# Kernel optimization log

Measured on AMD Instinct MI355X. Metric: run time of the kernel, lower is better.

Reference implementation:

```python
import jax, jax.numpy as jnp
import numpy as np
import math

L, B, T, S, D, H = 6, 4, 1024, 1024, 1024, 16
HD = D // H
SCALE = 1.0 / math.sqrt(HD)
EPS = 1e-5


def _ln(x, w, b):
    m = x.mean(-1, keepdims=True)
    v = ((x - m) ** 2).mean(-1, keepdims=True)
    return (x - m) * jax.lax.rsqrt(v + EPS) * w + b


def _mha(xq, xkv, qw, qb, kw, kb, vw, vb, ow, ob, mask):
    b, t, _ = xq.shape
    s = xkv.shape[1]
    q = (xq @ qw.T + qb).reshape(b, t, H, HD).transpose(0, 2, 1, 3)
    k = (xkv @ kw.T + kb).reshape(b, s, H, HD).transpose(0, 2, 1, 3)
    v = (xkv @ vw.T + vb).reshape(b, s, H, HD).transpose(0, 2, 1, 3)
    scores = jnp.einsum('bhqd,bhkd->bhqk', q, k) * SCALE
    scores = jnp.where(mask == 0, -jnp.inf, scores)
    attn = jax.nn.softmax(scores, axis=-1)  # dropout is identity (eval)
    o = jnp.einsum('bhqk,bhkd->bhqd', attn, v).transpose(0, 2, 1, 3).reshape(b, t, D)
    return o @ ow.T + ob


def _ffn(x, f1w, f1b, f2w, f2b, fnw, fnb):
    h = jax.nn.gelu(x @ f1w.T + f1b, approximate=False)
    y = h @ f2w.T + f2b
    return x + _ln(y, fnw, fnb)


def setup_inputs() -> dict:
    key = jax.random.key(0)
    ks = jax.random.split(key, 16)
    wf = lambda k: jax.random.normal(k, (L, D, D), jnp.float32) * 0.02
    zb = jnp.zeros((L, D), jnp.float32)
    ones = jnp.ones((L, D), jnp.float32)
    inp = {
        'x': jax.random.normal(ks[0], (B, T, D), jnp.float32),
        'enc_outputs': jax.random.normal(ks[1], (B, S, D), jnp.float32),
        'sqw': wf(ks[2]), 'sqb': zb, 'skw': wf(ks[3]), 'skb': zb,
        'svw': wf(ks[4]), 'svb': zb, 'sow': wf(ks[5]), 'sob': zb,
        'cqw': wf(ks[6]), 'cqb': zb, 'ckw': wf(ks[7]), 'ckb': zb,
        'cvw': wf(ks[8]), 'cvb': zb, 'cow': wf(ks[9]), 'cob': zb,
        'f1w': wf(ks[10]), 'f1b': zb, 'f2w': wf(ks[11]), 'f2b': zb,
        'fnw': ones, 'fnb': zb,
        'l1w': ones, 'l1b': zb, 'l2w': ones, 'l2b': zb, 'l3w': ones, 'l3b': zb,
        'src_mask': jnp.ones((1, 1, T, S), jnp.int32),
        'tgt_mask': jnp.tril(jnp.ones((T, T), jnp.int32))[None, None],
    }
    return inp


def reference(x, enc_outputs, sqw, sqb, skw, skb, svw, svb, sow, sob,
              cqw, cqb, ckw, ckb, cvw, cvb, cow, cob,
              f1w, f1b, f2w, f2b, fnw, fnb,
              l1w, l1b, l2w, l2b, l3w, l3b, src_mask, tgt_mask):
    for l in range(L):
        sa = _mha(x, x, sqw[l], sqb[l], skw[l], skb[l], svw[l], svb[l], sow[l], sob[l], tgt_mask)
        x = _ln(x + sa, l1w[l], l1b[l])
        ca = _mha(x, enc_outputs, cqw[l], cqb[l], ckw[l], ckb[l], cvw[l], cvb[l], cow[l], cob[l], src_mask)
        x = _ln(x + ca, l2w[l], l2b[l])
        ff = _ffn(x, f1w[l], f1b[l], f2w[l], f2b[l], fnw[l], fnb[l])
        x = _ln(x + ff, l3w[l], l3b[l])
    return x
```

## Files before the change

kernel.cpp:

```cpp
#include <hip/hip_runtime.h>
#include <stdint.h>

typedef unsigned short u16;
typedef unsigned int u32;
typedef __bf16 bf16x8 __attribute__((ext_vector_type(8)));
typedef float f32x4 __attribute__((ext_vector_type(4)));
typedef u16 u16x8 __attribute__((ext_vector_type(8)));
typedef u16 u16x4 __attribute__((ext_vector_type(4)));
typedef u32 u32x2 __attribute__((ext_vector_type(2)));

#define MFMA16(A, B, C) __builtin_amdgcn_mfma_f32_16x16x32_bf16((A), (B), (C), 0, 0, 0)

#define GLOAD_LDS16(GP, LP)                                                    \
  __builtin_amdgcn_global_load_lds(                                            \
      (__attribute__((address_space(1))) void*)(GP),                           \
      (__attribute__((address_space(3))) void*)(LP), 16, 0, 0)

__device__ __forceinline__ u16 f2bf(float f) {
  return __builtin_bit_cast(u16, (__bf16)f);
}

__device__ __forceinline__ float bf2f(u16 v) {
  return __builtin_bit_cast(float, ((u32)v) << 16);
}

__device__ __forceinline__ float exp2_raw(float x) {
  float r;
  asm("v_exp_f32 %0, %1\n\ts_nop 0" : "=v"(r) : "v"(x));
  return r;
}

__device__ __forceinline__ float max3f(float a, float b, float c) {
  float d;
  asm("v_max3_f32 %0, %1, %2, %3" : "=v"(d) : "v"(a), "v"(b), "v"(c));
  return d;
}

__device__ __forceinline__ u32 cvt_pk_bf16(float lo, float hi) {
  u32 r;
  asm("v_cvt_pk_bf16_f32 %0, %1, %2" : "=v"(r) : "v"(lo), "v"(hi));
  return r;
}

#define SC2 0.1803368801111204f
#define DEFER_THR 11.541560327f

struct WPtrs {
  const float* p[10];
};

__global__ __launch_bounds__(256) void wcvt_kernel(WPtrs w, u16* __restrict__ dst, int loff) {
  const int mat = blockIdx.y;
  const int i = blockIdx.x * 256 + threadIdx.x;
  float4 v = ((const float4*)(w.p[mat] + loff))[i];
  u16x4 o = {f2bf(v.x), f2bf(v.y), f2bf(v.z), f2bf(v.w)};
  ((u16x4*)dst)[(size_t)mat * gridDim.x * 256 + i] = o;
}

struct GemmArgs {
  const u16* A[3];
  const u16* W[3];
  const float* bias[3];
  u16* C[3];
  float scale[3];
};

__global__ __launch_bounds__(256, 4) void gemm_bt(GemmArgs g) {
  const int mat = blockIdx.y >> 3;
  const int n0 = (blockIdx.y & 7) * 128;
  const int m0 = blockIdx.x * 128;
  const int kz = blockIdx.z;
  const int kn = 16 / gridDim.z;
  const u16* __restrict__ A = g.A[mat];
  const u16* __restrict__ W = g.W[mat];

  __shared__ u16 As[128][64];
  __shared__ u16 Bs[128][64];

  const int tid = threadIdx.x;
  const int lane = tid & 63;
  const int wv = tid >> 6;
  const int wm = (wv >> 1) * 64;
  const int wn = (wv & 1) * 64;
  const int fr = lane & 15;
  const int fg = lane >> 4;

  f32x4 acc[4][4];
#pragma unroll
  for (int i = 0; i < 4; ++i)
#pragma unroll
    for (int j = 0; j < 4; ++j)
#pragma unroll
      for (int r = 0; r < 4; ++r) acc[i][j][r] = 0.f;

  const int row8 = lane >> 3;
  const int csw = ((lane & 7) ^ row8) * 8;
  const u16* ga = A + (size_t)(m0 + wv * 32 + row8) * 1024 + csw + kz * kn * 64;
  const u16* gb = W + (size_t)(n0 + wv * 32 + row8) * 1024 + csw + kz * kn * 64;

  for (int kt = 0; kt < kn; ++kt) {
    __syncthreads();
#pragma unroll
    for (int i = 0; i < 4; ++i) {
      GLOAD_LDS16(ga + (size_t)i * 8 * 1024, &As[wv * 32 + i * 8][0]);
      GLOAD_LDS16(gb + (size_t)i * 8 * 1024, &Bs[wv * 32 + i * 8][0]);
    }
    ga += 64;
    gb += 64;
    __syncthreads();
#pragma unroll
    for (int ks = 0; ks < 2; ++ks) {
      bf16x8 af[4], bfr[4];
#pragma unroll
      for (int i = 0; i < 4; ++i) {
        af[i] = *(const bf16x8*)&As[wm + i * 16 + fr][((ks * 4 + fg) ^ (fr & 7)) * 8];
        bfr[i] = *(const bf16x8*)&Bs[wn + i * 16 + fr][((ks * 4 + fg) ^ (fr & 7)) * 8];
      }
#pragma unroll
      for (int mi = 0; mi < 4; ++mi)
#pragma unroll
        for (int ni = 0; ni < 4; ++ni) acc[mi][ni] = MFMA16(af[mi], bfr[ni], acc[mi][ni]);
    }
  }

  const float* __restrict__ bias = g.bias[mat];
  const float scl = g.scale[mat];
  float bv[4];
#pragma unroll
  for (int ni = 0; ni < 4; ++ni) bv[ni] = (kz == 0) ? bias[n0 + wn + ni * 16 + fr] : 0.f;

  u16* __restrict__ C = g.C[mat] + (size_t)kz * (4096 * 1024);
#pragma unroll
  for (int mi = 0; mi < 4; ++mi) {
#pragma unroll
    for (int ni = 0; ni < 4; ++ni) {
      const int col = n0 + wn + ni * 16 + fr;
#pragma unroll
      for (int r = 0; r < 4; ++r) {
        const int row = m0 + wm + mi * 16 + fg * 4 + r;
        C[(size_t)row * 1024 + col] = f2bf((acc[mi][ni][r] + bv[ni]) * scl);
      }
    }
  }
}

__global__ __launch_bounds__(512, 4) void attn_fwd(const u16* __restrict__ Q,
                                                   const u16* __restrict__ K,
                                                   const u16* __restrict__ V,
                                                   u16* __restrict__ O, int causal) {
  const int b = blockIdx.x >> 4;
  const int h = blockIdx.x & 15;
  const int qb = causal ? (7 - blockIdx.y) : blockIdx.y;
  const int tid = threadIdx.x;
  const int lane = tid & 63;
  const int wv = tid >> 6;
  const int fr = lane & 15;
  const int fg = lane >> 4;

  __shared__ u16 Ks[2][64][64];
  __shared__ u16 Vt[2][64][64];
  __shared__ u16 Plds[8][16][64];

  const int qrow0 = b * 1024 + qb * 128 + wv * 16;
  const int col0 = h * 64;

  const u16* qp = Q + (size_t)(qrow0 + fr) * 1024 + col0 + fg * 8;
  bf16x8 aQ0 = *(const bf16x8*)qp;
  bf16x8 aQ1 = *(const bf16x8*)(qp + 32);

  f32x4 ov[4];
#pragma unroll
  for (int i = 0; i < 4; ++i)
#pragma unroll
    for (int r = 0; r < 4; ++r) ov[i][r] = 0.f;
  float m_run = -1e30f, l_part = 0.f;

  const int kv_base = b * 1024;
  const int qg = qb * 128 + wv * 16 + fr;
  const int nt = causal ? (2 * qb + 2) : 16;

  const u16* gk0 = K + (size_t)(kv_base + wv * 16 + (lane >> 3)) * 1024 + col0 +
                   (((lane & 7) ^ (lane >> 3)) * 8);
  const int vt = tid - 256;
  const int kkp = vt & 31;
  const int d0 = (vt >> 5) * 8;
  const u16* gv0 = V + (size_t)(kv_base + 2 * kkp) * 1024 + col0 + d0;

#define STAGE_K(T, BUF)                                                        \
  if (wv < 4) {                                                                \
    const u16* gk = gk0 + (size_t)(T)*64 * 1024;                               \
    GLOAD_LDS16(gk, &Ks[BUF][wv * 16][0]);                                     \
    GLOAD_LDS16(gk + 8 * 1024, &Ks[BUF][wv * 16 + 8][0]);                      \
  }
#define LOAD_V(T)                                                              \
  if (tid >= 256) {                                                            \
    const u16* gvp = gv0 + (size_t)(T)*64 * 1024;                              \
    vr0 = *(const u16x8*)gvp;                                                  \
    vr1 = *(const u16x8*)(gvp + 1024);                                         \
  }
#define WRITE_V(BUF)                                                           \
  if (tid >= 256) {                                                            \
    _Pragma("unroll") for (int j = 0; j < 8; ++j) {                            \
      u32 pk = (u32)vr0[j] | ((u32)vr1[j] << 16);                              \
      *(u32*)&Vt[BUF][d0 + j][(((kkp >> 2) ^ j) * 8) + (kkp & 3) * 2] = pk;    \
    }                                                                          \
  }

  u16x8 vr0, vr1;
  STAGE_K(0, 0);
  LOAD_V(0);
  WRITE_V(0);

  for (int t = 0; t < nt; ++t) {
    const int cur = t & 1;
    __syncthreads();
    const bool pf = (t + 1 < nt);
    if (pf) {
      STAGE_K(t + 1, cur ^ 1);
      LOAD_V(t + 1);
    }

    f32x4 st[4];
    __builtin_amdgcn_s_setprio(1);
#pragma unroll
    for (int hh = 0; hh < 4; ++hh) {
#pragma unroll
      for (int r = 0; r < 4; ++r) st[hh][r] = 0.f;
      const u16* krow = &Ks[cur][hh * 16 + fr][0];
      bf16x8 k0 = *(const bf16x8*)(krow + ((fg ^ (fr & 7)) * 8));
      bf16x8 k1 = *(const bf16x8*)(krow + (((4 + fg) ^ (fr & 7)) * 8));
      st[hh] = MFMA16(k0, aQ0, st[hh]);
      st[hh] = MFMA16(k1, aQ1, st[hh]);
    }
    __builtin_amdgcn_s_setprio(0);

    if (causal && t >= 2 * qb) {
#pragma unroll
      for (int hh = 0; hh < 4; ++hh)
#pragma unroll
        for (int r = 0; r < 4; ++r) {
          const int kkg = t * 64 + hh * 16 + fg * 4 + r;
          if (kkg > qg) st[hh][r] = -1e30f;
        }
    }

    float a = max3f(st[0][0], st[0][1], st[0][2]);
    a = max3f(a, st[0][3], st[1][0]);
    a = max3f(a, st[1][1], st[1][2]);
    a = max3f(a, st[1][3], st[2][0]);
    float bb = max3f(st[2][1], st[2][2], st[2][3]);
    bb = max3f(bb, st[3][0], st[3][1]);
    bb = max3f(bb, st[3][2], st[3][3]);
    const float tmax = fmaxf(a, bb);

    if (!__all(tmax <= m_run + DEFER_THR)) {
      float cm = fmaxf(tmax, __shfl_xor(tmax, 16));
      cm = fmaxf(cm, __shfl_xor(cm, 32));
      const float mnew = fmaxf(m_run, cm);
      const float fsc = exp2_raw(m_run - mnew);
      l_part *= fsc;
      float frs[4];
#pragma unroll
      for (int r = 0; r < 4; ++r) frs[r] = __shfl(fsc, fg * 4 + r);
#pragma unroll
      for (int dt = 0; dt < 4; ++dt)
#pragma unroll
        for (int r = 0; r < 4; ++r) ov[dt][r] *= frs[r];
      m_run = mnew;
    }

    float p[16];
#pragma unroll
    for (int hh = 0; hh < 4; ++hh)
#pragma unroll
      for (int r = 0; r < 4; ++r) {
        const float e = exp2_raw(st[hh][r] - m_run);
        p[hh * 4 + r] = e;
        l_part += e;
      }

#pragma unroll
    for (int hh = 0; hh < 4; ++hh) {
      u32x2 wpair = {cvt_pk_bf16(p[hh * 4 + 0], p[hh * 4 + 1]),
                     cvt_pk_bf16(p[hh * 4 + 2], p[hh * 4 + 3])};
      const int c = hh * 2 + (fg >> 1);
      *(u32x2*)&Plds[wv][fr][((c ^ (fr & 7)) * 8) + (fg & 1) * 4] = wpair;
    }
    bf16x8 pa[2];
#pragma unroll
    for (int ks = 0; ks < 2; ++ks)
      pa[ks] = *(const bf16x8*)&Plds[wv][fr][(((ks * 4 + fg) ^ (fr & 7)) * 8)];
    __builtin_amdgcn_s_setprio(1);
#pragma unroll
    for (int dt = 0; dt < 4; ++dt) {
#pragma unroll
      for (int ks = 0; ks < 2; ++ks) {
        bf16x8 bvv = *(const bf16x8*)&Vt[cur][dt * 16 + fr][(((ks * 4 + fg) ^ (fr & 7)) * 8)];
        ov[dt] = MFMA16(pa[ks], bvv, ov[dt]);
      }
    }
    __builtin_amdgcn_s_setprio(0);

    if (pf) WRITE_V(cur ^ 1);
  }

  float ps = l_part;
  ps += __shfl_xor(ps, 16);
  ps += __shfl_xor(ps, 32);
  const float linv = 1.0f / ps;
  float fin[4];
#pragma unroll
  for (int r = 0; r < 4; ++r) fin[r] = __shfl(linv, fg * 4 + r);
#pragma unroll
  for (int dt = 0; dt < 4; ++dt)
#pragma unroll
    for (int r = 0; r < 4; ++r) {
      const int row = qrow0 + fg * 4 + r;
      const int col = col0 + dt * 16 + fr;
      O[(size_t)row * 1024 + col] = f2bf(ov[dt][r] * fin[r]);
    }
#undef STAGE_K
#undef LOAD_V
#undef WRITE_V
}

__device__ __forceinline__ float4 ld_bf4(const u16* p, size_t idx4) {
  u16x4 t = ((const u16x4*)p)[idx4];
  return make_float4(bf2f(t[0]), bf2f(t[1]), bf2f(t[2]), bf2f(t[3]));
}

__global__ __launch_bounds__(256) void ln_res_kernel(const u16* __restrict__ Xb_in,
                                                     const u16* __restrict__ T0,
                                                     const u16* __restrict__ T1, int nT,
                                                     const float* __restrict__ w,
                                                     const float* __restrict__ bia,
                                                     u16* __restrict__ Xb_out) {
  __shared__ float red[2][4];
  const int row = blockIdx.x;
  const int tid = threadIdx.x;
  const int lane = tid & 63, wv = tid >> 6;
  const size_t base4 = (size_t)row * 256;
  float4 xv = ld_bf4(Xb_in, base4 + tid);
  float4 tv = ld_bf4(T0, base4 + tid);
  float z0 = xv.x + tv.x, z1 = xv.y + tv.y, z2 = xv.z + tv.z, z3 = xv.w + tv.w;
  if (nT == 2) {
    float4 t1 = ld_bf4(T1, base4 + tid);
    z0 += t1.x; z1 += t1.y; z2 += t1.z; z3 += t1.w;
  }
  float s = z0 + z1 + z2 + z3;
  float ss = z0 * z0 + z1 * z1 + z2 * z2 + z3 * z3;
#pragma unroll
  for (int m = 1; m <= 32; m <<= 1) {
    s += __shfl_xor(s, m);
    ss += __shfl_xor(ss, m);
  }
  if (lane == 0) {
    red[0][wv] = s;
    red[1][wv] = ss;
  }
  __syncthreads();
  s = red[0][0] + red[0][1] + red[0][2] + red[0][3];
  ss = red[1][0] + red[1][1] + red[1][2] + red[1][3];
  const float mean = s * (1.f / 1024.f);
  const float var = ss * (1.f / 1024.f) - mean * mean;
  const float rs = rsqrtf(fmaxf(var, 0.f) + 1e-5f);
  float4 wv4 = ((const float4*)w)[tid];
  float4 bv4 = ((const float4*)bia)[tid];
  float o0 = (z0 - mean) * rs * wv4.x + bv4.x;
  float o1 = (z1 - mean) * rs * wv4.y + bv4.y;
  float o2 = (z2 - mean) * rs * wv4.z + bv4.z;
  float o3 = (z3 - mean) * rs * wv4.w + bv4.w;
  u16x4 ob = {f2bf(o0), f2bf(o1), f2bf(o2), f2bf(o3)};
  ((u16x4*)Xb_out)[base4 + tid] = ob;
}

__global__ __launch_bounds__(256) void ffn_ln_kernel(
    const u16* __restrict__ Xb, const u16* __restrict__ Y0, const u16* __restrict__ Y1,
    int nT, const float* __restrict__ fw_, const float* __restrict__ fb_,
    const float* __restrict__ w3, const float* __restrict__ b3, u16* __restrict__ Xb_out,
    float* __restrict__ Fout) {
  __shared__ float red[2][4];
  const int row = blockIdx.x;
  const int tid = threadIdx.x;
  const int lane = tid & 63, wv = tid >> 6;
  const size_t base4 = (size_t)row * 256;
  float4 yv = ld_bf4(Y0, base4 + tid);
  if (nT == 2) {
    float4 y1 = ld_bf4(Y1, base4 + tid);
    yv.x += y1.x; yv.y += y1.y; yv.z += y1.z; yv.w += y1.w;
  }
  float s = yv.x + yv.y + yv.z + yv.w;
  float ss = yv.x * yv.x + yv.y * yv.y + yv.z * yv.z + yv.w * yv.w;
#pragma unroll
  for (int m = 1; m <= 32; m <<= 1) {
    s += __shfl_xor(s, m);
    ss += __shfl_xor(ss, m);
  }
  if (lane == 0) {
    red[0][wv] = s;
    red[1][wv] = ss;
  }
  __syncthreads();
  s = red[0][0] + red[0][1] + red[0][2] + red[0][3];
  ss = red[1][0] + red[1][1] + red[1][2] + red[1][3];
  const float mean = s * (1.f / 1024.f);
  const float var = ss * (1.f / 1024.f) - mean * mean;
  const float rs = rsqrtf(fmaxf(var, 0.f) + 1e-5f);
  float4 xv = ld_bf4(Xb, base4 + tid);
  float4 fw4 = ((const float4*)fw_)[tid];
  float4 fb4 = ((const float4*)fb_)[tid];
  float z0 = 2.f * xv.x + (yv.x - mean) * rs * fw4.x + fb4.x;
  float z1 = 2.f * xv.y + (yv.y - mean) * rs * fw4.y + fb4.y;
  float z2 = 2.f * xv.z + (yv.z - mean) * rs * fw4.z + fb4.z;
  float z3 = 2.f * xv.w + (yv.w - mean) * rs * fw4.w + fb4.w;
  float s2 = z0 + z1 + z2 + z3;
  float ss2 = z0 * z0 + z1 * z1 + z2 * z2 + z3 * z3;
#pragma unroll
  for (int m = 1; m <= 32; m <<= 1) {
    s2 += __shfl_xor(s2, m);
    ss2 += __shfl_xor(ss2, m);
  }
  __syncthreads();
  if (lane == 0) {
    red[0][wv] = s2;
    red[1][wv] = ss2;
  }
  __syncthreads();
  s2 = red[0][0] + red[0][1] + red[0][2] + red[0][3];
  ss2 = red[1][0] + red[1][1] + red[1][2] + red[1][3];
  const float mean2 = s2 * (1.f / 1024.f);
  const float var2 = ss2 * (1.f / 1024.f) - mean2 * mean2;
  const float rs2 = rsqrtf(fmaxf(var2, 0.f) + 1e-5f);
  float4 w4 = ((const float4*)w3)[tid];
  float4 b4 = ((const float4*)b3)[tid];
  float o0 = (z0 - mean2) * rs2 * w4.x + b4.x;
  float o1 = (z1 - mean2) * rs2 * w4.y + b4.y;
  float o2 = (z2 - mean2) * rs2 * w4.z + b4.z;
  float o3 = (z3 - mean2) * rs2 * w4.w + b4.w;
  u16x4 ob = {f2bf(o0), f2bf(o1), f2bf(o2), f2bf(o3)};
  ((u16x4*)Xb_out)[base4 + tid] = ob;
  if (Fout) ((float4*)Fout)[base4 + tid] = make_float4(o0, o1, o2, o3);
}

__global__ __launch_bounds__(256) void gelu_combine(const u16* __restrict__ T0,
                                                    const u16* __restrict__ T1, int nT,
                                                    u16* __restrict__ dst) {
  const size_t i = (size_t)blockIdx.x * 256 + threadIdx.x;
  float4 v = ld_bf4(T0, i);
  if (nT == 2) {
    float4 u = ld_bf4(T1, i);
    v.x += u.x; v.y += u.y; v.z += u.z; v.w += u.w;
  }
  v.x = 0.5f * v.x * (1.0f + erff(v.x * 0.70710678118654752f));
  v.y = 0.5f * v.y * (1.0f + erff(v.y * 0.70710678118654752f));
  v.z = 0.5f * v.z * (1.0f + erff(v.z * 0.70710678118654752f));
  v.w = 0.5f * v.w * (1.0f + erff(v.w * 0.70710678118654752f));
  u16x4 o = {f2bf(v.x), f2bf(v.y), f2bf(v.z), f2bf(v.w)};
  ((u16x4*)dst)[i] = o;
}

__global__ __launch_bounds__(256) void cast_kernel(const float* __restrict__ in,
                                                   u16* __restrict__ outb) {
  const size_t i = (size_t)blockIdx.x * 256 + threadIdx.x;
  float4 v = ((const float4*)in)[i];
  u16x4 o = {f2bf(v.x), f2bf(v.y), f2bf(v.z), f2bf(v.w)};
  ((u16x4*)outb)[i] = o;
}

extern "C" void kernel_launch(void* const* d_in, const int* in_sizes, int n_in, void* d_out,
                              int out_size, void* d_ws, size_t ws_size, hipStream_t stream) {
  const float* x_in = (const float*)d_in[0];
  const float* enc = (const float*)d_in[1];
  const float* sqw = (const float*)d_in[2];
  const float* sqb = (const float*)d_in[3];
  const float* skw = (const float*)d_in[4];
  const float* skb = (const float*)d_in[5];
  const float* svw = (const float*)d_in[6];
  const float* svb = (const float*)d_in[7];
  const float* sow = (const float*)d_in[8];
  const float* sob = (const float*)d_in[9];
  const float* cqw = (const float*)d_in[10];
  const float* cqb = (const float*)d_in[11];
  const float* ckw = (const float*)d_in[12];
  const float* ckb = (const float*)d_in[13];
  const float* cvw = (const float*)d_in[14];
  const float* cvb = (const float*)d_in[15];
  const float* cow = (const float*)d_in[16];
  const float* cob = (const float*)d_in[17];
  const float* f1w = (const float*)d_in[18];
  const float* f1b = (const float*)d_in[19];
  const float* f2w = (const float*)d_in[20];
  const float* f2b = (const float*)d_in[21];
  const float* fnw = (const float*)d_in[22];
  const float* fnb = (const float*)d_in[23];
  const float* l1w = (const float*)d_in[24];
  const float* l1b = (const float*)d_in[25];
  const float* l2w = (const float*)d_in[26];
  const float* l2b = (const float*)d_in[27];
  const float* l3w = (const float*)d_in[28];
  const float* l3b = (const float*)d_in[29];

  const size_t MB = 1024 * 1024;
  const int ALLW = (ws_size >= 200 * MB) ? 1 : 0;
  const int NS = (ws_size >= 90 * MB) ? 2 : 1;
  char* ws = (char*)d_ws;
  u16* tmpb = (u16*)ws;
  char* p = ws + (size_t)NS * 8 * MB;
  u16* xb = (u16*)p;   p += 8 * MB;
  u16* encb = (u16*)p; p += 8 * MB;
  u16* qbuf = (u16*)p; p += 8 * MB;
  u16* kbuf = (u16*)p; p += 8 * MB;
  u16* vbuf = (u16*)p; p += 8 * MB;
  u16* wbf = (u16*)p;
  u16* tmpb1 = tmpb + (size_t)4 * 1024 * 1024;
  const size_t W1M = 1024 * 1024;

  cast_kernel<<<4096, 256, 0, stream>>>(x_in, xb);
  cast_kernel<<<4096, 256, 0, stream>>>(enc, encb);

  WPtrs wp;
  wp.p[0] = sqw; wp.p[1] = skw; wp.p[2] = svw; wp.p[3] = sow;
  wp.p[4] = cqw; wp.p[5] = ckw; wp.p[6] = cvw; wp.p[7] = cow;
  wp.p[8] = f1w; wp.p[9] = f2w;

  if (ALLW) wcvt_kernel<<<dim3(6144, 10), 256, 0, stream>>>(wp, wbf, 0);

  for (int l = 0; l < 6; ++l) {
    const size_t bo = (size_t)l * 1024;
    if (!ALLW) wcvt_kernel<<<dim3(1024, 10), 256, 0, stream>>>(wp, wbf, l * (int)W1M);
    #define WT(t) (ALLW ? (wbf + ((size_t)(t)*6 + l) * W1M) : (wbf + (size_t)(t)*W1M))

    GemmArgs g;
    g.scale[0] = SC2; g.scale[1] = 1.f; g.scale[2] = 1.f;
    g.A[0] = xb; g.A[1] = xb; g.A[2] = xb;
    g.W[0] = WT(0); g.W[1] = WT(1); g.W[2] = WT(2);
    g.bias[0] = sqb + bo; g.bias[1] = skb + bo; g.bias[2] = svb + bo;
    g.C[0] = qbuf; g.C[1] = kbuf; g.C[2] = vbuf;
    gemm_bt<<<dim3(32, 24, 1), 256, 0, stream>>>(g);
    attn_fwd<<<dim3(64, 8), 512, 0, stream>>>(qbuf, kbuf, vbuf, qbuf, 1);
    g.scale[0] = 1.f;
    g.A[0] = qbuf; g.W[0] = WT(3); g.bias[0] = sob + bo; g.C[0] = tmpb;
    gemm_bt<<<dim3(32, 8, NS), 256, 0, stream>>>(g);
    ln_res_kernel<<<4096, 256, 0, stream>>>(xb, tmpb, tmpb1, NS, l1w + bo, l1b + bo, xb);

    g.scale[0] = SC2;
    g.A[0] = xb; g.A[1] = encb; g.A[2] = encb;
    g.W[0] = WT(4); g.W[1] = WT(5); g.W[2] = WT(6);
    g.bias[0] = cqb + bo; g.bias[1] = ckb + bo; g.bias[2] = cvb + bo;
    g.C[0] = qbuf; g.C[1] = kbuf; g.C[2] = vbuf;
    gemm_bt<<<dim3(32, 24, 1), 256, 0, stream>>>(g);
    attn_fwd<<<dim3(64, 8), 512, 0, stream>>>(qbuf, kbuf, vbuf, qbuf, 0);
    g.scale[0] = 1.f;
    g.A[0] = qbuf; g.W[0] = WT(7); g.bias[0] = cob + bo; g.C[0] = tmpb;
    gemm_bt<<<dim3(32, 8, NS), 256, 0, stream>>>(g);
    ln_res_kernel<<<4096, 256, 0, stream>>>(xb, tmpb, tmpb1, NS, l2w + bo, l2b + bo, xb);

    g.A[0] = xb; g.W[0] = WT(8); g.bias[0] = f1b + bo; g.C[0] = tmpb;
    gemm_bt<<<dim3(32, 8, NS), 256, 0, stream>>>(g);
    gelu_combine<<<4096, 256, 0, stream>>>(tmpb, tmpb1, NS, kbuf);
    g.A[0] = kbuf; g.W[0] = WT(9); g.bias[0] = f2b + bo; g.C[0] = tmpb;
    gemm_bt<<<dim3(32, 8, NS), 256, 0, stream>>>(g);
    float* fo = (l == 5) ? (float*)d_out : nullptr;
    ffn_ln_kernel<<<4096, 256, 0, stream>>>(xb, tmpb, tmpb1, NS, fnw + bo, fnb + bo, l3w + bo,
                                            l3b + bo, xb, fo);
    #undef WT
  }
}
```

Before: 1.352 ms.

## Rework attention to 4 waves of 32 query rows using 32x32 MFMA for QK^T

The attention kernel now runs 256 threads (4 waves), each wave owning 32 query rows instead of 16. QK^T uses the 32x32x16 bf16 MFMA, and each V fragment read from LDS feeds two 16x16 MFMAs, which halves LDS traffic per FLOP and drops the shuffle-based row max across lane groups. All threads now share K and V staging, and launch bounds change to (256,3). The weight-cast kernel is also widened to convert 16 floats per thread with fewer blocks. The cost is higher register pressure per wave and fewer waves in flight to hide latency.

```diff
diff --git a/kernel.cpp b/kernel.cpp
--- a/kernel.cpp
+++ b/kernel.cpp
@@ -5,11 +5,13 @@
 typedef unsigned int u32;
 typedef __bf16 bf16x8 __attribute__((ext_vector_type(8)));
 typedef float f32x4 __attribute__((ext_vector_type(4)));
+typedef float f32x16 __attribute__((ext_vector_type(16)));
 typedef u16 u16x8 __attribute__((ext_vector_type(8)));
 typedef u16 u16x4 __attribute__((ext_vector_type(4)));
 typedef u32 u32x2 __attribute__((ext_vector_type(2)));
 
 #define MFMA16(A, B, C) __builtin_amdgcn_mfma_f32_16x16x32_bf16((A), (B), (C), 0, 0, 0)
+#define MFMA32(A, B, C) __builtin_amdgcn_mfma_f32_32x32x16_bf16((A), (B), (C), 0, 0, 0)
 
 #define GLOAD_LDS16(GP, LP)                                                    \
   __builtin_amdgcn_global_load_lds(                                            \
@@ -51,10 +53,16 @@
 
 __global__ __launch_bounds__(256) void wcvt_kernel(WPtrs w, u16* __restrict__ dst, int loff) {
   const int mat = blockIdx.y;
-  const int i = blockIdx.x * 256 + threadIdx.x;
-  float4 v = ((const float4*)(w.p[mat] + loff))[i];
-  u16x4 o = {f2bf(v.x), f2bf(v.y), f2bf(v.z), f2bf(v.w)};
-  ((u16x4*)dst)[(size_t)mat * gridDim.x * 256 + i] = o;
+  const size_t t = (size_t)blockIdx.x * 256 + threadIdx.x;
+  const float4* src = (const float4*)(w.p[mat] + loff) + t * 4;
+  float4 v0 = src[0], v1 = src[1], v2 = src[2], v3 = src[3];
+  u16x8 o0 = {f2bf(v0.x), f2bf(v0.y), f2bf(v0.z), f2bf(v0.w),
+              f2bf(v1.x), f2bf(v1.y), f2bf(v1.z), f2bf(v1.w)};
+  u16x8 o1 = {f2bf(v2.x), f2bf(v2.y), f2bf(v2.z), f2bf(v2.w),
+              f2bf(v3.x), f2bf(v3.y), f2bf(v3.z), f2bf(v3.w)};
+  u16x8* d = (u16x8*)dst + (size_t)mat * gridDim.x * 512 + t * 2;
+  d[0] = o0;
+  d[1] = o1;
 }
 
 struct GemmArgs {
@@ -144,7 +152,7 @@
   }
 }
 
-__global__ __launch_bounds__(512, 4) void attn_fwd(const u16* __restrict__ Q,
+__global__ __launch_bounds__(256, 3) void attn_fwd(const u16* __restrict__ Q,
                                                    const u16* __restrict__ K,
                                                    const u16* __restrict__ V,
                                                    u16* __restrict__ O, int causal) {
@@ -156,50 +164,54 @@
   const int wv = tid >> 6;
   const int fr = lane & 15;
   const int fg = lane >> 4;
+  const int lq = lane & 31;
+  const int hi = lane >> 5;
 
   __shared__ u16 Ks[2][64][64];
   __shared__ u16 Vt[2][64][64];
-  __shared__ u16 Plds[8][16][64];
-
-  const int qrow0 = b * 1024 + qb * 128 + wv * 16;
+  __shared__ u16 Plds[4][32][64];
+
+  const int qrow0 = b * 1024 + qb * 128 + wv * 32;
   const int col0 = h * 64;
 
-  const u16* qp = Q + (size_t)(qrow0 + fr) * 1024 + col0 + fg * 8;
-  bf16x8 aQ0 = *(const bf16x8*)qp;
-  bf16x8 aQ1 = *(const bf16x8*)(qp + 32);
-
-  f32x4 ov[4];
-#pragma unroll
-  for (int i = 0; i < 4; ++i)
-#pragma unroll
-    for (int r = 0; r < 4; ++r) ov[i][r] = 0.f;
+  const u16* qp = Q + (size_t)(qrow0 + lq) * 1024 + col0 + hi * 8;
+  bf16x8 aQ[4];
+#pragma unroll
+  for (int seg = 0; seg < 4; ++seg) aQ[seg] = *(const bf16x8*)(qp + seg * 16);
+
+  f32x4 ov[2][4];
+#pragma unroll
+  for (int qh = 0; qh < 2; ++qh)
+#pragma unroll
+    for (int i = 0; i < 4; ++i)
+#pragma unroll
+      for (int r = 0; r < 4; ++r) ov[qh][i][r] = 0.f;
   float m_run = -1e30f, l_part = 0.f;
 
   const int kv_base = b * 1024;
-  const int qg = qb * 128 + wv * 16 + fr;
+  const int qg = qb * 128 + wv * 32 + lq;
   const int nt = causal ? (2 * qb + 2) : 16;
 
   const u16* gk0 = K + (size_t)(kv_base + wv * 16 + (lane >> 3)) * 1024 + col0 +
                    (((lane & 7) ^ (lane >> 3)) * 8);
-  const int vt = tid - 256;
-  const int kkp = vt & 31;
-  const int d0 = (vt >> 5) * 8;
+  const int kkp = tid & 31;
+  const int d0 = (tid >> 5) * 8;
   const u16* gv0 = V + (size_t)(kv_base + 2 * kkp) * 1024 + col0 + d0;
 
 #define STAGE_K(T, BUF)                                                        \
-  if (wv < 4) {                                                                \
+  {                                                                            \
     const u16* gk = gk0 + (size_t)(T)*64 * 1024;                               \
     GLOAD_LDS16(gk, &Ks[BUF][wv * 16][0]);                                     \
     GLOAD_LDS16(gk + 8 * 1024, &Ks[BUF][wv * 16 + 8][0]);                      \
   }
 #define LOAD_V(T)                                                              \
-  if (tid >= 256) {                                                            \
+  {                                                                            \
     const u16* gvp = gv0 + (size_t)(T)*64 * 1024;                              \
     vr0 = *(const u16x8*)gvp;                                                  \
     vr1 = *(const u16x8*)(gvp + 1024);                                         \
   }
 #define WRITE_V(BUF)                                                           \
-  if (tid >= 256) {                                                            \
+  {                                                                            \
     _Pragma("unroll") for (int j = 0; j < 8; ++j) {                            \
       u32 pk = (u32)vr0[j] | ((u32)vr1[j] << 16);                              \
       *(u32*)&Vt[BUF][d0 + j][(((kkp >> 2) ^ j) * 8) + (kkp & 3) * 2] = pk;    \
@@ -220,105 +232,106 @@
       LOAD_V(t + 1);
     }
 
-    f32x4 st[4];
+    f32x16 st[2];
     __builtin_amdgcn_s_setprio(1);
 #pragma unroll
-    for (int hh = 0; hh < 4; ++hh) {
-#pragma unroll
-      for (int r = 0; r < 4; ++r) st[hh][r] = 0.f;
-      const u16* krow = &Ks[cur][hh * 16 + fr][0];
-      bf16x8 k0 = *(const bf16x8*)(krow + ((fg ^ (fr & 7)) * 8));
-      bf16x8 k1 = *(const bf16x8*)(krow + (((4 + fg) ^ (fr & 7)) * 8));
-      st[hh] = MFMA16(k0, aQ0, st[hh]);
-      st[hh] = MFMA16(k1, aQ1, st[hh]);
+    for (int kb2 = 0; kb2 < 2; ++kb2) {
+#pragma unroll
+      for (int r = 0; r < 16; ++r) st[kb2][r] = 0.f;
+#pragma unroll
+      for (int seg = 0; seg < 4; ++seg) {
+        bf16x8 ka = *(const bf16x8*)&Ks[cur][kb2 * 32 + lq][((seg * 2 + hi) ^ (lq & 7)) * 8];
+        st[kb2] = MFMA32(ka, aQ[seg], st[kb2]);
+      }
     }
     __builtin_amdgcn_s_setprio(0);
 
     if (causal && t >= 2 * qb) {
 #pragma unroll
-      for (int hh = 0; hh < 4; ++hh)
-#pragma unroll
-        for (int r = 0; r < 4; ++r) {
-          const int kkg = t * 64 + hh * 16 + fg * 4 + r;
-          if (kkg > qg) st[hh][r] = -1e30f;
+      for (int kb2 = 0; kb2 < 2; ++kb2)
+#pragma unroll
+        for (int r = 0; r < 16; ++r) {
+          const int kkg = t * 64 + kb2 * 32 + (r & 3) + 8 * (r >> 2) + 4 * hi;
+          if (kkg > qg) st[kb2][r] = -1e30f;
         }
     }
 
-    float a = max3f(st[0][0], st[0][1], st[0][2]);
-    a = max3f(a, st[0][3], st[1][0]);
-    a = max3f(a, st[1][1], st[1][2]);
-    a = max3f(a, st[1][3], st[2][0]);
-    float bb = max3f(st[2][1], st[2][2], st[2][3]);
-    bb = max3f(bb, st[3][0], st[3][1]);
-    bb = max3f(bb, st[3][2], st[3][3]);
-    const float tmax = fmaxf(a, bb);
-
-    if (!__all(tmax <= m_run + DEFER_THR)) {
-      float cm = fmaxf(tmax, __shfl_xor(tmax, 16));
-      cm = fmaxf(cm, __shfl_xor(cm, 32));
-      const float mnew = fmaxf(m_run, cm);
+    float tA = st[0][0];
+#pragma unroll
+    for (int r = 1; r < 15; r += 2) tA = max3f(tA, st[0][r], st[0][r + 1]);
+    tA = fmaxf(tA, st[0][15]);
+    float tB = st[1][0];
+#pragma unroll
+    for (int r = 1; r < 15; r += 2) tB = max3f(tB, st[1][r], st[1][r + 1]);
+    tB = fmaxf(tB, st[1][15]);
+    const float tq = fmaxf(fmaxf(tA, tB), __shfl_xor(fmaxf(tA, tB), 32));
+
+    if (!__all(tq <= m_run + DEFER_THR)) {
+      const float mnew = fmaxf(m_run, tq);
       const float fsc = exp2_raw(m_run - mnew);
       l_part *= fsc;
-      float frs[4];
-#pragma unroll
-      for (int r = 0; r < 4; ++r) frs[r] = __shfl(fsc, fg * 4 + r);
-#pragma unroll
-      for (int dt = 0; dt < 4; ++dt)
-#pragma unroll
-        for (int r = 0; r < 4; ++r) ov[dt][r] *= frs[r];
+#pragma unroll
+      for (int qh = 0; qh < 2; ++qh) {
+        float frs[4];
+#pragma unroll
+        for (int r = 0; r < 4; ++r) frs[r] = __shfl(fsc, qh * 16 + fg * 4 + r);
+#pragma unroll
+        for (int dt = 0; dt < 4; ++dt)
+#pragma unroll
+          for (int r = 0; r < 4; ++r) ov[qh][dt][r] *= frs[r];
+      }
       m_run = mnew;
     }
 
-    float p[16];
-#pragma unroll
-    for (int hh = 0; hh < 4; ++hh)
+#pragma unroll
+    for (int kb2 = 0; kb2 < 2; ++kb2) {
+#pragma unroll
+      for (int j = 0; j < 8; ++j) {
+        const int r0 = 2 * j;
+        const float e0 = exp2_raw(st[kb2][r0] - m_run);
+        const float e1 = exp2_raw(st[kb2][r0 + 1] - m_run);
+        l_part += e0 + e1;
+        const int kk0 = kb2 * 32 + (r0 & 3) + 8 * (r0 >> 2) + 4 * hi;
+        const int idx = (((kk0 >> 3) ^ (lq & 7)) * 8) + (kk0 & 7);
+        *(u32*)&Plds[wv][lq][idx] = cvt_pk_bf16(e0, e1);
+      }
+    }
+
+    __builtin_amdgcn_s_setprio(1);
+#pragma unroll
+    for (int seg = 0; seg < 2; ++seg) {
+      bf16x8 paq[2];
+#pragma unroll
+      for (int qh = 0; qh < 2; ++qh)
+        paq[qh] = *(const bf16x8*)&Plds[wv][qh * 16 + fr][(((seg * 4 + fg) ^ (fr & 7)) * 8)];
+#pragma unroll
+      for (int dt = 0; dt < 4; ++dt) {
+        bf16x8 bvv = *(const bf16x8*)&Vt[cur][dt * 16 + fr][(((seg * 4 + fg) ^ (fr & 7)) * 8)];
+        ov[0][dt] = MFMA16(paq[0], bvv, ov[0][dt]);
+        ov[1][dt] = MFMA16(paq[1], bvv, ov[1][dt]);
+      }
+    }
+    __builtin_amdgcn_s_setprio(0);
+
+    if (pf) WRITE_V(cur ^ 1);
+  }
+
+  float ps = l_part + __shfl_xor(l_part, 32);
+  const float linv = 1.0f / ps;
+#pragma unroll
+  for (int qh = 0; qh < 2; ++qh) {
+    float fin[4];
+#pragma unroll
+    for (int r = 0; r < 4; ++r) fin[r] = __shfl(linv, qh * 16 + fg * 4 + r);
+#pragma unroll
+    for (int dt = 0; dt < 4; ++dt)
 #pragma unroll
       for (int r = 0; r < 4; ++r) {
-        const float e = exp2_raw(st[hh][r] - m_run);
-        p[hh * 4 + r] = e;
-        l_part += e;
-      }
-
-#pragma unroll
-    for (int hh = 0; hh < 4; ++hh) {
-      u32x2 wpair = {cvt_pk_bf16(p[hh * 4 + 0], p[hh * 4 + 1]),
-                     cvt_pk_bf16(p[hh * 4 + 2], p[hh * 4 + 3])};
-      const int c = hh * 2 + (fg >> 1);
-      *(u32x2*)&Plds[wv][fr][((c ^ (fr & 7)) * 8) + (fg & 1) * 4] = wpair;
-    }
-    bf16x8 pa[2];
-#pragma unroll
-    for (int ks = 0; ks < 2; ++ks)
-      pa[ks] = *(const bf16x8*)&Plds[wv][fr][(((ks * 4 + fg) ^ (fr & 7)) * 8)];
-    __builtin_amdgcn_s_setprio(1);
-#pragma unroll
-    for (int dt = 0; dt < 4; ++dt) {
-#pragma unroll
-      for (int ks = 0; ks < 2; ++ks) {
-        bf16x8 bvv = *(const bf16x8*)&Vt[cur][dt * 16 + fr][(((ks * 4 + fg) ^ (fr & 7)) * 8)];
-        ov[dt] = MFMA16(pa[ks], bvv, ov[dt]);
-      }
-    }
-    __builtin_amdgcn_s_setprio(0);
-
-    if (pf) WRITE_V(cur ^ 1);
-  }
-
-  float ps = l_part;
-  ps += __shfl_xor(ps, 16);
-  ps += __shfl_xor(ps, 32);
-  const float linv = 1.0f / ps;
-  float fin[4];
-#pragma unroll
-  for (int r = 0; r < 4; ++r) fin[r] = __shfl(linv, fg * 4 + r);
-#pragma unroll
-  for (int dt = 0; dt < 4; ++dt)
-#pragma unroll
-    for (int r = 0; r < 4; ++r) {
-      const int row = qrow0 + fg * 4 + r;
-      const int col = col0 + dt * 16 + fr;
-      O[(size_t)row * 1024 + col] = f2bf(ov[dt][r] * fin[r]);
-    }
+        const int row = qrow0 + qh * 16 + fg * 4 + r;
+        const int col = col0 + dt * 16 + fr;
+        O[(size_t)row * 1024 + col] = f2bf(ov[qh][dt][r] * fin[r]);
+      }
+  }
 #undef STAGE_K
 #undef LOAD_V
 #undef WRITE_V
@@ -523,11 +536,11 @@
   wp.p[4] = cqw; wp.p[5] = ckw; wp.p[6] = cvw; wp.p[7] = cow;
   wp.p[8] = f1w; wp.p[9] = f2w;
 
-  if (ALLW) wcvt_kernel<<<dim3(6144, 10), 256, 0, stream>>>(wp, wbf, 0);
+  if (ALLW) wcvt_kernel<<<dim3(1536, 10), 256, 0, stream>>>(wp, wbf, 0);
 
   for (int l = 0; l < 6; ++l) {
     const size_t bo = (size_t)l * 1024;
-    if (!ALLW) wcvt_kernel<<<dim3(1024, 10), 256, 0, stream>>>(wp, wbf, l * (int)W1M);
+    if (!ALLW) wcvt_kernel<<<dim3(256, 10), 256, 0, stream>>>(wp, wbf, l * (int)W1M);
     #define WT(t) (ALLW ? (wbf + ((size_t)(t)*6 + l) * W1M) : (wbf + (size_t)(t)*W1M))
 
     GemmArgs g;
@@ -537,7 +550,7 @@
     g.bias[0] = sqb + bo; g.bias[1] = skb + bo; g.bias[2] = svb + bo;
     g.C[0] = qbuf; g.C[1] = kbuf; g.C[2] = vbuf;
     gemm_bt<<<dim3(32, 24, 1), 256, 0, stream>>>(g);
-    attn_fwd<<<dim3(64, 8), 512, 0, stream>>>(qbuf, kbuf, vbuf, qbuf, 1);
+    attn_fwd<<<dim3(64, 8), 256, 0, stream>>>(qbuf, kbuf, vbuf, qbuf, 1);
     g.scale[0] = 1.f;
     g.A[0] = qbuf; g.W[0] = WT(3); g.bias[0] = sob + bo; g.C[0] = tmpb;
     gemm_bt<<<dim3(32, 8, NS), 256, 0, stream>>>(g);
@@ -549,7 +562,7 @@
     g.bias[0] = cqb + bo; g.bias[1] = ckb + bo; g.bias[2] = cvb + bo;
     g.C[0] = qbuf; g.C[1] = kbuf; g.C[2] = vbuf;
     gemm_bt<<<dim3(32, 24, 1), 256, 0, stream>>>(g);
-    attn_fwd<<<dim3(64, 8), 512, 0, stream>>>(qbuf, kbuf, vbuf, qbuf, 0);
+    attn_fwd<<<dim3(64, 8), 256, 0, stream>>>(qbuf, kbuf, vbuf, qbuf, 0);
     g.scale[0] = 1.f;
     g.A[0] = qbuf; g.W[0] = WT(7); g.bias[0] = cob + bo; g.C[0] = tmpb;
     gemm_bt<<<dim3(32, 8, NS), 256, 0, stream>>>(g);
```

Measured after the change: 1.413 ms. +4.5%, slower.
